# Performance work log

Hardware: AMD Instinct MI355X
Metric: run time of the kernel (lower is better)

Reference implementation:

```python
import jax, jax.numpy as jnp
import numpy as np

CENTER_EXTEND_PX = 3.0  # center_extend_px
SIGMA = 2.0             # center_gt_blur
KSIZE = 21              # GaussianLayer: ReflectionPad2d(10) + 21x21 depthwise gaussian
PAD = KSIZE // 2


def _gaussian_kernel():
    ax = np.arange(KSIZE, dtype=np.float64) - PAD
    xx, yy = np.meshgrid(ax, ax)
    g = np.exp(-(xx ** 2 + yy ** 2) / (2.0 * SIGMA ** 2))
    g /= g.sum()
    return jnp.asarray(g, dtype=jnp.float32)


def _blur(x, kernel):
    # x: [H, W]; reflect-pad then VALID depthwise conv == GaussianLayer
    xp = jnp.pad(x, PAD, mode='reflect')
    return jax.lax.conv_general_dilated(xp[None, None], kernel[None, None], (1, 1), 'VALID')[0, 0]


def setup_inputs():
    key = jax.random.key(0)
    B, N, H, W = 4, 64, 512, 512
    kc = jax.random.fold_in(key, 1)
    # centers[b, n] = (y, x) pixel coordinates; >0 means valid
    centers = jax.random.randint(kc, (B, N, 2), 1, min(H, W)).astype(jnp.float32)
    centerdir_gt = jnp.zeros((B, 6, H, W), dtype=jnp.float32)
    return {"centers": centers, "centerdir_gt": centerdir_gt, "kernel": _gaussian_kernel()}


def reference(centers, centerdir_gt, kernel):
    B, _, H, W = centerdir_gt.shape
    # xym grid: xym[0] varies along width, xym[1] varies along height (integer coords)
    grid_h = jnp.arange(H, dtype=jnp.float32)[:, None]  # xym[1]: [H,1]
    grid_w = jnp.arange(W, dtype=jnp.float32)[None, :]  # xym[0]: [1,W]

    def per_item(c, gt_b):
        valid = (c[:, 0] > 0) | (c[:, 1] > 0)          # [N]
        cy, cx = c[:, 0], c[:, 1]
        # original: X = xym[1] (height grid) paired with center_x = centers[:,1]
        dx = grid_h[:, :, None] - cx                    # [H,1,N]
        dy = grid_w[:, :, None] - cy                    # [1,W,N]
        d2 = dx * dx + dy * dy                          # [H,W,N]; squared dist (same argmin as sqrt)
        d2 = jnp.where(valid[None, None, :], d2, jnp.inf)
        ids = jnp.argmin(d2, axis=-1)                   # [H,W] nearest valid center per pixel
        gt_X = cx[ids] - grid_h                         # [H,W]
        gt_Y = cy[ids] - grid_w
        r2 = gt_X * gt_X + gt_Y * gt_Y
        gt_R = jnp.where(r2 > 0, jnp.sqrt(jnp.where(r2 > 0, r2, 1.0)), 0.0)
        gt_theta = jnp.arctan2(gt_Y, jnp.where(r2 > 0, gt_X, 1.0))  # atan2(0,1)=0 == atan2(0,0)
        s, co = jnp.sin(gt_theta), jnp.cos(gt_theta)
        M = jnp.sqrt(s * s + co * co)
        s, co = s / M, co / M
        near = (jnp.abs(gt_X) < CENTER_EXTEND_PX) & (jnp.abs(gt_Y) < CENTER_EXTEND_PX)
        has_valid = valid.any()
        mask0 = jnp.where(has_valid, near.astype(jnp.float32), 0.0)  # == 1 - gt_center_mask
        blurred = _blur(mask0, kernel)
        m = blurred.max()
        center_mask = jnp.where(mask0.max() > 0, blurred / jnp.maximum(m, 1e-12), 0.0)
        ch = jnp.where(has_valid, jnp.stack([gt_R, gt_theta, s, co]), gt_b[:4])
        return jnp.concatenate([ch, gt_b[4:5], center_mask[None]], axis=0)  # [6,H,W]

    return jax.vmap(per_item)(centers, centerdir_gt)
```

## Files before the change

### kernel.cpp

```cpp
#include <hip/hip_runtime.h>
#include <math.h>
#include <limits.h>

namespace {
constexpr int BB   = 4;
constexpr int NCH  = 6;
constexpr int HH   = 512;
constexpr int WW   = 512;
constexpr int NCEN = 64;
constexpr int KSZ  = 21;
constexpr int PADR = 10;
constexpr int HW   = HH * WW;
constexpr int SENT = -1024;
constexpr int BOXSTRIDE = 640;

__device__ __forceinline__ int refl(int q, int n) {
    q = (q < 0) ? -q : q;
    q = (q >= n) ? (2 * n - 2 - q) : q;
    return q;
}

__global__ __launch_bounds__(256) void k_geom(
    const float* __restrict__ centers,
    const float* __restrict__ gt,
    float* __restrict__ out,
    float* __restrict__ mask,
    unsigned int* __restrict__ maxbuf)
{
    __shared__ int2  s_cen[2][NCEN];
    __shared__ float s_cxf[NCEN], s_cyf[NCEN];
    __shared__ int   s_has;

    const int b   = blockIdx.y;
    const int tid = threadIdx.x;
    const int r0  = blockIdx.x * 2;

    if (blockIdx.x == 0 && tid == 0) maxbuf[b] = 0u;
    if (tid == 0) s_has = 0;
    __syncthreads();
    if (tid < NCEN) {
        float cy = centers[(b * NCEN + tid) * 2 + 0];
        float cx = centers[(b * NCEN + tid) * 2 + 1];
        bool valid = (cy > 0.0f) || (cx > 0.0f);
        if (valid) atomicOr(&s_has, 1);
        s_cyf[tid] = cy;
        s_cxf[tid] = cx;
        int icx = valid ? (int)cx : SENT;
        int icy = valid ? (int)cy : SENT;
        int dx0 = r0 - icx;
        int dx1 = r0 + 1 - icx;
        s_cen[0][tid] = make_int2(icy * 8, 64 * dx0 * dx0 + tid);
        s_cen[1][tid] = make_int2(icy * 8, 64 * dx1 * dx1 + tid);
    }
    __syncthreads();

    const int rr  = tid >> 7;
    const int w0  = (tid & 127) * 4;
    const int row = r0 + rr;
    const int idx0 = row * WW + w0;

    const int iw8_0 = (w0 + 0) * 8;
    const int iw8_1 = (w0 + 1) * 8;
    const int iw8_2 = (w0 + 2) * 8;
    const int iw8_3 = (w0 + 3) * 8;
    int b0 = INT_MAX, b1 = INT_MAX, b2 = INT_MAX, b3 = INT_MAX;

    const int2* cen = s_cen[rr];
#pragma unroll 8
    for (int i = 0; i < NCEN; ++i) {
        int2 c = cen[i];
        int d0 = iw8_0 - c.x; b0 = min(b0, __mul24(d0, d0) + c.y);
        int d1 = iw8_1 - c.x; b1 = min(b1, __mul24(d1, d1) + c.y);
        int d2 = iw8_2 - c.x; b2 = min(b2, __mul24(d2, d2) + c.y);
        int d3 = iw8_3 - c.x; b3 = min(b3, __mul24(d3, d3) + c.y);
    }
    int bi[4] = { b0 & 63, b1 & 63, b2 & 63, b3 & 63 };

    const bool hv = (s_has != 0);
    float aR[4], aT[4], aS[4], aC[4], aM[4];
    const float fh = (float)row;
#pragma unroll
    for (int j = 0; j < 4; ++j) {
        float cxw = s_cxf[bi[j]];
        float cyw = s_cyf[bi[j]];
        float gX = cxw - fh;
        float gY = cyw - (float)(w0 + j);
        float r2 = gX * gX + gY * gY;
        bool rpos = r2 > 0.0f;
        float R = rpos ? sqrtf(r2) : 0.0f;
        aR[j] = R;
        aT[j] = atan2f(gY, rpos ? gX : 1.0f);
        float invR = rpos ? (1.0f / R) : 0.0f;
        aS[j] = rpos ? gY * invR : 0.0f;
        aC[j] = rpos ? gX * invR : 1.0f;
        bool nearc = (fabsf(gX) < 3.0f) && (fabsf(gY) < 3.0f);
        aM[j] = (hv && nearc) ? 1.0f : 0.0f;
    }

    const size_t base = (size_t)b * NCH * HW + (size_t)idx0;
    if (hv) {
        *(float4*)&out[base + 0 * (size_t)HW] = make_float4(aR[0], aR[1], aR[2], aR[3]);
        *(float4*)&out[base + 1 * (size_t)HW] = make_float4(aT[0], aT[1], aT[2], aT[3]);
        *(float4*)&out[base + 2 * (size_t)HW] = make_float4(aS[0], aS[1], aS[2], aS[3]);
        *(float4*)&out[base + 3 * (size_t)HW] = make_float4(aC[0], aC[1], aC[2], aC[3]);
    } else {
        *(float4*)&out[base + 0 * (size_t)HW] = *(const float4*)&gt[base + 0 * (size_t)HW];
        *(float4*)&out[base + 1 * (size_t)HW] = *(const float4*)&gt[base + 1 * (size_t)HW];
        *(float4*)&out[base + 2 * (size_t)HW] = *(const float4*)&gt[base + 2 * (size_t)HW];
        *(float4*)&out[base + 3 * (size_t)HW] = *(const float4*)&gt[base + 3 * (size_t)HW];
    }
    *(float4*)&out[base + 4 * (size_t)HW] = *(const float4*)&gt[base + 4 * (size_t)HW];
    *(float4*)&out[base + 5 * (size_t)HW] = make_float4(0.f, 0.f, 0.f, 0.f);
    *(float4*)&mask[(size_t)b * HW + idx0] = make_float4(aM[0], aM[1], aM[2], aM[3]);
}

__device__ __forceinline__ void load_k1(const float* __restrict__ g2d, float* k1) {
    if (threadIdx.x < KSZ) {
        float s = 0.0f;
#pragma unroll
        for (int j = 0; j < KSZ; ++j) s += g2d[threadIdx.x * KSZ + j];
        k1[threadIdx.x] = s;
    }
}

__global__ __launch_bounds__(256) void k_blur_sparse(
    const float* __restrict__ centers,
    const float* __restrict__ mask,
    const float* __restrict__ g2d,
    float* __restrict__ blurbox,
    unsigned int* __restrict__ maxbuf)
{
    const int b  = blockIdx.y;
    const int ci = blockIdx.x;
    float cy = centers[(b * NCEN + ci) * 2 + 0];
    float cx = centers[(b * NCEN + ci) * 2 + 1];
    if (!((cy > 0.0f) || (cx > 0.0f))) return;
    const int icx = (int)cx, icy = (int)cy;
    const int rA = max(icx - 12, 0), rB = min(icx + 12, HH - 1);
    const int cA = max(icy - 12, 0), cB = min(icy + 12, WW - 1);
    const int pr0 = max(rA - PADR, 0), pr1 = min(rB + PADR, HH - 1);
    const int pc0 = max(cA - PADR, 0), pc1 = min(cB + PADR, WW - 1);
    const int nr = pr1 - pr0 + 1, nc = pc1 - pc0 + 1;
    const int nh = rB - rA + 1,  nw = cB - cA + 1;

    __shared__ float k1[KSZ];
    __shared__ float patch[45 * 48];
    __shared__ float tmp[25 * 46];
    load_k1(g2d, k1);

    const float* mb = mask + (size_t)b * HW;
    for (int e = threadIdx.x; e < nr * nc; e += 256) {
        int r = e / nc, c = e - r * nc;
        patch[r * 48 + c] = mb[(pr0 + r) * WW + (pc0 + c)];
    }
    __syncthreads();

    for (int e = threadIdx.x; e < nh * nc; e += 256) {
        int lr = e / nc, j = e - lr * nc;
        int r  = rA + lr;
        float acc = 0.0f;
#pragma unroll
        for (int dv = -PADR; dv <= PADR; ++dv) {
            int q = refl(r + dv, HH);
            acc = fmaf(k1[dv + PADR], patch[(q - pr0) * 48 + j], acc);
        }
        tmp[lr * 46 + j] = acc;
    }
    __syncthreads();

    float vmax = 0.0f;
    float* bx = blurbox + (size_t)(b * NCEN + ci) * BOXSTRIDE;
    for (int e = threadIdx.x; e < nh * nw; e += 256) {
        int lr = e / nw, j = e - lr * nw;
        int w  = cA + j;
        float acc = 0.0f;
#pragma unroll
        for (int d = -PADR; d <= PADR; ++d) {
            int q = refl(w + d, WW);
            acc = fmaf(k1[d + PADR], tmp[lr * 46 + (q - pc0)], acc);
        }
        bx[lr * 25 + j] = acc;
        vmax = fmaxf(vmax, acc);
    }
#pragma unroll
    for (int off = 32; off > 0; off >>= 1)
        vmax = fmaxf(vmax, __shfl_down(vmax, off, 64));
    __shared__ float swr[4];
    const int lane = threadIdx.x & 63, wid = threadIdx.x >> 6;
    if (lane == 0) swr[wid] = vmax;
    __syncthreads();
    if (threadIdx.x == 0) {
        float m = fmaxf(fmaxf(swr[0], swr[1]), fmaxf(swr[2], swr[3]));
        atomicMax(&maxbuf[b], __float_as_uint(m));
    }
}

__global__ __launch_bounds__(256) void k_norm_sparse(
    const float* __restrict__ centers,
    const float* __restrict__ blurbox,
    const unsigned int* __restrict__ maxbuf,
    float* __restrict__ out)
{
    const int b  = blockIdx.y;
    const int ci = blockIdx.x;
    float cy = centers[(b * NCEN + ci) * 2 + 0];
    float cx = centers[(b * NCEN + ci) * 2 + 1];
    if (!((cy > 0.0f) || (cx > 0.0f))) return;
    const int icx = (int)cx, icy = (int)cy;
    const int rA = max(icx - 12, 0), rB = min(icx + 12, HH - 1);
    const int cA = max(icy - 12, 0), cB = min(icy + 12, WW - 1);
    const int nh = rB - rA + 1, nw = cB - cA + 1;

    const float inv = 1.0f / fmaxf(__uint_as_float(maxbuf[b]), 1e-12f);
    const float* bx = blurbox + (size_t)(b * NCEN + ci) * BOXSTRIDE;
    float* o5 = out + ((size_t)b * NCH + 5) * HW;
    for (int e = threadIdx.x; e < nh * nw; e += 256) {
        int lr = e / nw, j = e - lr * nw;
        o5[(rA + lr) * WW + (cA + j)] = bx[lr * 25 + j] * inv;
    }
}

}

extern "C" void kernel_launch(void* const* d_in, const int* in_sizes, int n_in,
                              void* d_out, int out_size, void* d_ws, size_t ws_size,
                              hipStream_t stream) {
    (void)in_sizes; (void)n_in; (void)out_size; (void)ws_size;
    const float* centers = (const float*)d_in[0];
    const float* gt      = (const float*)d_in[1];
    const float* g2d     = (const float*)d_in[2];
    float* out  = (float*)d_out;
    float* mask = (float*)d_ws;
    float* blurbox = (float*)d_ws + (size_t)BB * HW;
    unsigned int* maxbuf =
        (unsigned int*)((float*)d_ws + (size_t)BB * HW + (size_t)BB * NCEN * BOXSTRIDE);

    dim3 gridG(HW / 1024, BB);
    k_geom<<<gridG, 256, 0, stream>>>(centers, gt, out, mask, maxbuf);
    dim3 gridS(NCEN, BB);
    k_blur_sparse<<<gridS, 256, 0, stream>>>(centers, mask, g2d, blurbox, maxbuf);
    k_norm_sparse<<<gridS, 256, 0, stream>>>(centers, blurbox, maxbuf, out);
}
```

Measured before the change: 99.00 us.

## Cull nearest-center candidates per 32x32 tile and use polynomial atan2

The geometry kernel now processes 32x32 pixel tiles instead of two-row strips. For each tile it computes a lower and upper distance bound for every center and keeps only centers whose minimum distance can beat the best worst-case distance, so the per-pixel argmin loop runs over a short candidate list instead of all 64 centers. The library atan2f is also replaced by a minimax polynomial approximation, which cuts transcendental cost at the price of small angle error. Tile rows are 32 floats wide, so stores form shorter contiguous segments than the previous full-row layout.

```diff
diff --git a/kernel.cpp b/kernel.cpp
--- a/kernel.cpp
+++ b/kernel.cpp
@@ -11,13 +11,29 @@
 constexpr int KSZ  = 21;
 constexpr int PADR = 10;
 constexpr int HW   = HH * WW;
-constexpr int SENT = -1024;
 constexpr int BOXSTRIDE = 640;
 
 __device__ __forceinline__ int refl(int q, int n) {
     q = (q < 0) ? -q : q;
     q = (q >= n) ? (2 * n - 2 - q) : q;
     return q;
+}
+
+__device__ __forceinline__ float fast_atan2(float y, float x) {
+    float ax = fabsf(x), ay = fabsf(y);
+    float mx = fmaxf(ax, ay), mn = fminf(ax, ay);
+    float r = mn / mx;
+    float s = r * r;
+    float p = -0.0117212f;
+    p = fmaf(p, s, 0.05265332f);
+    p = fmaf(p, s, -0.11643287f);
+    p = fmaf(p, s, 0.19354346f);
+    p = fmaf(p, s, -0.33262347f);
+    p = fmaf(p, s, 0.99997726f);
+    float a = r * p;
+    a = (ay > ax) ? 1.57079632679489662f - a : a;
+    a = (x < 0.0f) ? 3.14159265358979323f - a : a;
+    return (y < 0.0f) ? -a : a;
 }
 
 __global__ __launch_bounds__(256) void k_geom(
@@ -27,56 +43,68 @@
     float* __restrict__ mask,
     unsigned int* __restrict__ maxbuf)
 {
-    __shared__ int2  s_cen[2][NCEN];
     __shared__ float s_cxf[NCEN], s_cyf[NCEN];
-    __shared__ int   s_has;
-
-    const int b   = blockIdx.y;
-    const int tid = threadIdx.x;
-    const int r0  = blockIdx.x * 2;
-
-    if (blockIdx.x == 0 && tid == 0) maxbuf[b] = 0u;
-    if (tid == 0) s_has = 0;
-    __syncthreads();
+    __shared__ int   s_kx[NCEN], s_ky8[NCEN], s_ki[NCEN];
+    __shared__ int   s_cnt, s_hasv;
+
+    const int b    = blockIdx.y;
+    const int tid  = threadIdx.x;
+    const int tIdx = blockIdx.x;
+    const int r0   = (tIdx >> 4) * 32;
+    const int c0   = (tIdx & 15) * 32;
+
+    if (tIdx == 0 && tid == 0) maxbuf[b] = 0u;
+
     if (tid < NCEN) {
         float cy = centers[(b * NCEN + tid) * 2 + 0];
         float cx = centers[(b * NCEN + tid) * 2 + 1];
         bool valid = (cy > 0.0f) || (cx > 0.0f);
-        if (valid) atomicOr(&s_has, 1);
+        s_cxf[tid] = cx;
         s_cyf[tid] = cy;
-        s_cxf[tid] = cx;
-        int icx = valid ? (int)cx : SENT;
-        int icy = valid ? (int)cy : SENT;
-        int dx0 = r0 - icx;
-        int dx1 = r0 + 1 - icx;
-        s_cen[0][tid] = make_int2(icy * 8, 64 * dx0 * dx0 + tid);
-        s_cen[1][tid] = make_int2(icy * 8, 64 * dx1 * dx1 + tid);
-    }
-    __syncthreads();
-
-    const int rr  = tid >> 7;
-    const int w0  = (tid & 127) * 4;
-    const int row = r0 + rr;
-    const int idx0 = row * WW + w0;
-
-    const int iw8_0 = (w0 + 0) * 8;
-    const int iw8_1 = (w0 + 1) * 8;
-    const int iw8_2 = (w0 + 2) * 8;
-    const int iw8_3 = (w0 + 3) * 8;
+        float r0f = (float)r0, r1f = (float)(r0 + 31);
+        float c0f = (float)c0, c1f = (float)(c0 + 31);
+        float drm = fmaxf(fmaxf(r0f - cx, cx - r1f), 0.0f);
+        float dcm = fmaxf(fmaxf(c0f - cy, cy - c1f), 0.0f);
+        float drM = fmaxf(cx - r0f, r1f - cx);
+        float dcM = fmaxf(cy - c0f, c1f - cy);
+        float mind2 = drm * drm + dcm * dcm;
+        float maxd2 = drM * drM + dcM * dcM;
+        if (!valid) { mind2 = __int_as_float(0x7f800000); maxd2 = mind2; }
+        float ub = maxd2;
+#pragma unroll
+        for (int off = 32; off > 0; off >>= 1)
+            ub = fminf(ub, __shfl_xor(ub, off, 64));
+        bool keep = valid && (mind2 <= ub);
+        unsigned long long km = __ballot(keep);
+        unsigned long long vm = __ballot(valid);
+        if (keep) {
+            int pos = __popcll(km & ((1ull << tid) - 1ull));
+            s_kx[pos]  = (int)cx;
+            s_ky8[pos] = ((int)cy) * 8;
+            s_ki[pos]  = tid;
+        }
+        if (tid == 0) { s_cnt = (int)__popcll(km); s_hasv = (vm != 0ull) ? 1 : 0; }
+    }
+    __syncthreads();
+
+    const int row = r0 + (tid >> 3);
+    const int wb  = c0 + (tid & 7) * 4;
+    const int w8  = wb * 8;
+    const int cnt = s_cnt;
+    const bool hv = (s_hasv != 0);
+
     int b0 = INT_MAX, b1 = INT_MAX, b2 = INT_MAX, b3 = INT_MAX;
-
-    const int2* cen = s_cen[rr];
-#pragma unroll 8
-    for (int i = 0; i < NCEN; ++i) {
-        int2 c = cen[i];
-        int d0 = iw8_0 - c.x; b0 = min(b0, __mul24(d0, d0) + c.y);
-        int d1 = iw8_1 - c.x; b1 = min(b1, __mul24(d1, d1) + c.y);
-        int d2 = iw8_2 - c.x; b2 = min(b2, __mul24(d2, d2) + c.y);
-        int d3 = iw8_3 - c.x; b3 = min(b3, __mul24(d3, d3) + c.y);
+    for (int k = 0; k < cnt; ++k) {
+        int dr   = row - s_kx[k];
+        int base = (__mul24(dr, dr) << 6) + s_ki[k];
+        int icy8 = s_ky8[k];
+        int d0 = w8      - icy8; b0 = min(b0, __mul24(d0, d0) + base);
+        int d1 = w8 + 8  - icy8; b1 = min(b1, __mul24(d1, d1) + base);
+        int d2 = w8 + 16 - icy8; b2 = min(b2, __mul24(d2, d2) + base);
+        int d3 = w8 + 24 - icy8; b3 = min(b3, __mul24(d3, d3) + base);
     }
     int bi[4] = { b0 & 63, b1 & 63, b2 & 63, b3 & 63 };
 
-    const bool hv = (s_has != 0);
     float aR[4], aT[4], aS[4], aC[4], aM[4];
     const float fh = (float)row;
 #pragma unroll
@@ -84,12 +112,12 @@
         float cxw = s_cxf[bi[j]];
         float cyw = s_cyf[bi[j]];
         float gX = cxw - fh;
-        float gY = cyw - (float)(w0 + j);
+        float gY = cyw - (float)(wb + j);
         float r2 = gX * gX + gY * gY;
         bool rpos = r2 > 0.0f;
         float R = rpos ? sqrtf(r2) : 0.0f;
         aR[j] = R;
-        aT[j] = atan2f(gY, rpos ? gX : 1.0f);
+        aT[j] = fast_atan2(gY, rpos ? gX : 1.0f);
         float invR = rpos ? (1.0f / R) : 0.0f;
         aS[j] = rpos ? gY * invR : 0.0f;
         aC[j] = rpos ? gX * invR : 1.0f;
@@ -97,7 +125,7 @@
         aM[j] = (hv && nearc) ? 1.0f : 0.0f;
     }
 
-    const size_t base = (size_t)b * NCH * HW + (size_t)idx0;
+    const size_t base = (size_t)b * NCH * HW + (size_t)(row * WW + wb);
     if (hv) {
         *(float4*)&out[base + 0 * (size_t)HW] = make_float4(aR[0], aR[1], aR[2], aR[3]);
         *(float4*)&out[base + 1 * (size_t)HW] = make_float4(aT[0], aT[1], aT[2], aT[3]);
@@ -111,7 +139,8 @@
     }
     *(float4*)&out[base + 4 * (size_t)HW] = *(const float4*)&gt[base + 4 * (size_t)HW];
     *(float4*)&out[base + 5 * (size_t)HW] = make_float4(0.f, 0.f, 0.f, 0.f);
-    *(float4*)&mask[(size_t)b * HW + idx0] = make_float4(aM[0], aM[1], aM[2], aM[3]);
+    *(float4*)&mask[(size_t)b * HW + (size_t)(row * WW + wb)] =
+        make_float4(aM[0], aM[1], aM[2], aM[3]);
 }
 
 __device__ __forceinline__ void load_k1(const float* __restrict__ g2d, float* k1) {
@@ -235,7 +264,7 @@
     unsigned int* maxbuf =
         (unsigned int*)((float*)d_ws + (size_t)BB * HW + (size_t)BB * NCEN * BOXSTRIDE);
 
-    dim3 gridG(HW / 1024, BB);
+    dim3 gridG(256, BB);
     k_geom<<<gridG, 256, 0, stream>>>(centers, gt, out, mask, maxbuf);
     dim3 gridS(NCEN, BB);
     k_blur_sparse<<<gridS, 256, 0, stream>>>(centers, mask, g2d, blurbox, maxbuf);
```

After: 94.84 us. 1.04x faster.
